# Performance work log

Measured on AMD Instinct MI355X. Metric: run time of the kernel, lower is better.

Reference implementation:

```python
import jax, jax.numpy as jnp
import numpy as np

N_TOKENS = 4096
EMBED = 2048
D_ATTN = 2048


def setup_inputs() -> dict:
    key = jax.random.key(0)
    k1, k2, k3, k4 = jax.random.split(key, 4)
    # torch.rand -> uniform [0,1); keeps scores positive so the multiplicative
    # -inf mask acts as a clean causal mask (faithful to original behavior).
    token_embeddings = jax.random.uniform(k1, (N_TOKENS, EMBED), dtype=jnp.float32)
    W_Q = jax.random.uniform(k2, (EMBED, D_ATTN), dtype=jnp.float32)
    W_K = jax.random.uniform(k3, (EMBED, D_ATTN), dtype=jnp.float32)
    W_V = jax.random.uniform(k4, (EMBED, D_ATTN), dtype=jnp.float32)
    return {"token_embeddings": token_embeddings, "W_Q": W_Q, "W_K": W_K, "W_V": W_V}


def reference(token_embeddings, W_Q, W_K, W_V):
    n = token_embeddings.shape[0]
    d = W_Q.shape[1]
    # mask: 1 on/below diagonal, -inf strictly above (multiplicative, as in source)
    neg_inf = jnp.float32(-jnp.inf)
    mask = jnp.tril(jnp.ones((n, n), dtype=jnp.float32)) + jnp.triu(
        jnp.full((n, n), neg_inf, dtype=jnp.float32), k=1
    )
    Q = token_embeddings @ W_Q          # (n, d)
    K = token_embeddings @ W_K          # (n, d)
    V = token_embeddings @ W_V          # (n, d)
    scores = (Q @ K.T) * mask           # (n, n); upper tri -> -inf (scores > 0)
    scores = scores / jnp.sqrt(jnp.float32(d))
    attn = jax.nn.softmax(scores, axis=-1)
    return attn @ V                     # (n, d)
```

## Files before the change

### kernel.cpp

```cpp
#include <hip/hip_runtime.h>
#include <hip/hip_bf16.h>
#include <cstdint>
#include <cstddef>
#include <cmath>

#define N_TOK 4096
#define EMB   2048
#define DATT  2048

typedef __attribute__((ext_vector_type(8))) short short8;
typedef __attribute__((ext_vector_type(4))) short shortx4;
typedef __attribute__((ext_vector_type(4))) float f32x4;

#define MFMA(a, b, c) __builtin_amdgcn_mfma_f32_16x16x32_bf16(a, b, c, 0, 0, 0)

__device__ __forceinline__ short f2bs(float f) {
  __hip_bfloat16 h = __float2bfloat16(f);
  return __builtin_bit_cast(short, h);
}
__device__ __forceinline__ float bs2f(short s) {
  return __uint_as_float(((unsigned)(unsigned short)s) << 16);
}
__device__ __forceinline__ float ldin(const void* p, size_t i, int isbf) {
  if (isbf) {
    unsigned short u = ((const unsigned short*)p)[i];
    return __uint_as_float(((unsigned int)u) << 16);
  }
  return ((const float*)p)[i];
}

__device__ __forceinline__ size_t swz(int r, int c, int kdim) {
  return ((size_t)((r >> 7) * (kdim >> 3) + (c >> 3)) << 10) +
         (size_t)((r & 127) << 3) + (c & 7);
}

__device__ __forceinline__ void gl16(const short* g, short* l) {
  __builtin_amdgcn_global_load_lds(
      (const __attribute__((address_space(1))) unsigned int*)(const void*)g,
      (__attribute__((address_space(3))) unsigned int*)(void*)l, 16, 0, 0);
}

template <bool THREE>
__device__ __forceinline__ void gemm_core(const short* Ah, const short* Al,
                                          const short* Bh, const short* Bl,
                                          int chunks, int apan, int bpan,
                                          int kmax, short* lds,
                                          f32x4 acc[4][4]) {
  const int NSL = THREE ? 4 : 2;
  int tid = threadIdx.x;
  int lane = tid & 63;
  int wave = tid >> 6;
  int ln = lane & 15, quad = lane >> 4;
  int wm = (wave >> 1) * 64, wn = (wave & 1) * 64;
  int wofs = wave * 512;

  auto stage = [&](int b, int k0) {
    size_t ao = ((size_t)(apan * chunks + (k0 >> 3))) << 10;
    size_t bo = ((size_t)(bpan * chunks + (k0 >> 3))) << 10;
    short* base = lds + b * NSL * 4096;
    const short* sa = Ah + ao + tid * 8;
    const short* sb = Bh + bo + tid * 8;
    gl16(sa,        base + wofs);
    gl16(sa + 2048, base + wofs + 2048);
    gl16(sb,        base + 4096 + wofs);
    gl16(sb + 2048, base + 4096 + wofs + 2048);
    if (THREE) {
      const short* sal = Al + ao + tid * 8;
      const short* sbl = Bl + bo + tid * 8;
      gl16(sal,        base + 8192 + wofs);
      gl16(sal + 2048, base + 8192 + wofs + 2048);
      gl16(sbl,        base + 12288 + wofs);
      gl16(sbl + 2048, base + 12288 + wofs + 2048);
    }
  };

  stage(0, 0);
  int cur = 0;
  int abase = quad * 1024 + (wm + ln) * 8;
  int bbase = quad * 1024 + (wn + ln) * 8;
  for (int k0 = 0; k0 < kmax; k0 += 32) {
    __syncthreads();
    if (k0 + 32 < kmax) stage(cur ^ 1, k0 + 32);
    const short* B0 = lds + cur * NSL * 4096;
    short8 fah[4], fbh[4];
#pragma unroll
    for (int i = 0; i < 4; ++i) fah[i] = *(const short8*)(B0 + abase + i * 128);
#pragma unroll
    for (int j = 0; j < 4; ++j) fbh[j] = *(const short8*)(B0 + 4096 + bbase + j * 128);
    if (THREE) {
      short8 fal[4], fbl[4];
#pragma unroll
      for (int i = 0; i < 4; ++i) fal[i] = *(const short8*)(B0 + 8192 + abase + i * 128);
#pragma unroll
      for (int j = 0; j < 4; ++j) fbl[j] = *(const short8*)(B0 + 12288 + bbase + j * 128);
#pragma unroll
      for (int j = 0; j < 4; ++j)
#pragma unroll
        for (int i = 0; i < 4; ++i) {
          acc[i][j] = MFMA(fah[i], fbh[j], acc[i][j]);
          acc[i][j] = MFMA(fah[i], fbl[j], acc[i][j]);
          acc[i][j] = MFMA(fal[i], fbh[j], acc[i][j]);
        }
    } else {
#pragma unroll
      for (int j = 0; j < 4; ++j)
#pragma unroll
        for (int i = 0; i < 4; ++i) acc[i][j] = MFMA(fah[i], fbh[j], acc[i][j]);
    }
    cur ^= 1;
  }
}

template <int AP, int BP>
__device__ __forceinline__ void gemm8(const short* __restrict__ Ah,
                                      const short* __restrict__ Al,
                                      const short* __restrict__ Bh,
                                      const short* __restrict__ Bl,
                                      int chunks, int apan, int bpan,
                                      int kmax, short* lds, f32x4 acc[4][4]) {
  constexpr int ASZ = AP * 4096;
  constexpr int BSZ = BP * 4096;
  constexpr int OAL = ASZ;
  constexpr int OBH = 2 * ASZ;
  constexpr int OBL = 2 * ASZ + BSZ;
  constexpr int BUF = 2 * ASZ + 2 * BSZ;
  constexpr int NNW = BP * 2;
  int tid = threadIdx.x;
  int lane = tid & 63, wave = tid >> 6;
  int ln = lane & 15, quad = lane >> 4;
  int wm = (wave / NNW) * 64, wn = (wave % NNW) * 64;
  int nt = kmax >> 5;

  auto sp = [&](int b, int t, int p) {
    short* base = lds + b * BUF;
    const short* g;
    short* l;
    if (p < AP)               { g = Ah + (((size_t)(apan + p) * chunks + (t << 2)) << 10);          l = base + p * 4096; }
    else if (p < 2 * AP)      { int q = p - AP;      g = Al + (((size_t)(apan + q) * chunks + (t << 2)) << 10); l = base + OAL + q * 4096; }
    else if (p < 2 * AP + BP) { int q = p - 2 * AP;  g = Bh + (((size_t)(bpan + q) * chunks + (t << 2)) << 10); l = base + OBH + q * 4096; }
    else                      { int q = p - 2 * AP - BP; g = Bl + (((size_t)(bpan + q) * chunks + (t << 2)) << 10); l = base + OBL + q * 4096; }
    gl16(g + tid * 8, l + wave * 512);
  };

#pragma unroll
  for (int p = 0; p < 6; ++p) sp(0, 0, p);
  if (nt > 1) {
#pragma unroll
    for (int p = 0; p < 6; ++p) sp(1, 1, p);
  }

  int abase = (wm & 128) * 32 + quad * 1024 + ((wm & 64) + ln) * 8;
  int bbase = (wn & 128) * 32 + quad * 1024 + ((wn & 64) + ln) * 8;
  int bi = 0;
  for (int t = 0; t < nt; ++t) {
    if (t + 1 < nt) asm volatile("s_waitcnt vmcnt(6)" ::: "memory");
    else            asm volatile("s_waitcnt vmcnt(0)" ::: "memory");
    __builtin_amdgcn_s_barrier();
    __builtin_amdgcn_sched_barrier(0);

    const short* L = lds + bi * BUF;
    int pi = bi + 2; if (pi > 2) pi -= 3;
    bool pf = (t + 2 < nt);

    short8 bh[4], bl[4];
#pragma unroll
    for (int j = 0; j < 4; ++j) {
      bh[j] = *(const short8*)(L + OBH + bbase + j * 128);
      bl[j] = *(const short8*)(L + OBL + bbase + j * 128);
    }
#pragma unroll
    for (int i = 0; i < 4; ++i) {
      short8 ah = *(const short8*)(L + abase + i * 128);
      short8 al = *(const short8*)(L + OAL + abase + i * 128);
      if (pf) {
        if (i == 0)      { sp(pi, t + 2, 0); sp(pi, t + 2, 1); }
        else if (i == 1) { sp(pi, t + 2, 2); sp(pi, t + 2, 3); }
        else if (i == 2) { sp(pi, t + 2, 4); }
        else             { sp(pi, t + 2, 5); }
      }
      __builtin_amdgcn_s_setprio(1);
#pragma unroll
      for (int j = 0; j < 4; ++j) {
        acc[i][j] = MFMA(ah, bh[j], acc[i][j]);
        acc[i][j] = MFMA(ah, bl[j], acc[i][j]);
        acc[i][j] = MFMA(al, bh[j], acc[i][j]);
      }
      __builtin_amdgcn_s_setprio(0);
    }
    ++bi; if (bi > 2) bi = 0;
  }
}

__device__ __forceinline__ void gemm1d2(const short* __restrict__ Ah,
                                        const short* __restrict__ Bh,
                                        int chunks, int apan, int bpan,
                                        int kmax, short* lds, f32x4 acc[4][4]) {
  int tid = threadIdx.x;
  int lane = tid & 63, wave = tid >> 6;
  int ln = lane & 15, quad = lane >> 4;
  int wm = (wave >> 1) * 64, wn = (wave & 1) * 64;
  int wofs = wave * 512;
  int nt = kmax >> 5;

  auto stage = [&](int b, int t) {
    size_t ao = ((size_t)(apan * chunks + (t << 2))) << 10;
    size_t bo = ((size_t)(bpan * chunks + (t << 2))) << 10;
    short* base = lds + b * 8192;
    gl16(Ah + ao + tid * 8,        base + wofs);
    gl16(Ah + ao + 2048 + tid * 8, base + wofs + 2048);
    gl16(Bh + bo + tid * 8,        base + 4096 + wofs);
    gl16(Bh + bo + 2048 + tid * 8, base + 4096 + wofs + 2048);
  };
  stage(0, 0);
  if (nt > 1) stage(1, 1);

  int abase = quad * 1024 + (wm + ln) * 8;
  int bbase = quad * 1024 + (wn + ln) * 8;
  int bi = 0;
  for (int t = 0; t < nt; ++t) {
    if (t + 1 < nt) asm volatile("s_waitcnt vmcnt(4)" ::: "memory");
    else            asm volatile("s_waitcnt vmcnt(0)" ::: "memory");
    __builtin_amdgcn_s_barrier();
    __builtin_amdgcn_sched_barrier(0);
    int pi = bi + 2; if (pi > 2) pi -= 3;
    if (t + 2 < nt) stage(pi, t + 2);
    const short* L = lds + bi * 8192;
    short8 fah[4], fbh[4];
#pragma unroll
    for (int i = 0; i < 4; ++i) fah[i] = *(const short8*)(L + abase + i * 128);
#pragma unroll
    for (int j = 0; j < 4; ++j) fbh[j] = *(const short8*)(L + 4096 + bbase + j * 128);
#pragma unroll
    for (int j = 0; j < 4; ++j)
#pragma unroll
      for (int i = 0; i < 4; ++i) acc[i][j] = MFMA(fah[i], fbh[j], acc[i][j]);
    ++bi; if (bi > 2) bi = 0;
  }
}

__global__ void k_sniff(const void* x, int* flag) {
  if (threadIdx.x == 0 && blockIdx.x == 0) {
    const unsigned short* u = (const unsigned short*)x;
    int bf = 1;
    for (int i = 0; i < 256; ++i) {
      unsigned short v = u[i];
      if ((v & 0x8000u) || ((v & 0x7FFFu) >= 0x3F80u)) { bf = 0; break; }
    }
    *flag = bf;
  }
}

__global__ __launch_bounds__(256) void k_xbar(const void* X, float* xbar,
                                              const int* flagp) {
  int isbf = *flagp;
  int e = blockIdx.x * 256 + threadIdx.x;
  float s = 0.f;
  for (int r = 0; r < 256; ++r) s += ldin(X, (size_t)r * EMB + e, isbf);
  xbar[e] = s * (1.f / 256.f);
}

__global__ __launch_bounds__(256) void k_split_x(const void* X, short* Xh, short* Xl,
                                                 const int* flagp) {
  int isbf = *flagp;
  size_t base = ((size_t)blockIdx.x * 256 + threadIdx.x) * 4;
  int r = (int)(base >> 11), c = (int)(base & 2047);
  shortx4 h, l;
#pragma unroll
  for (int u = 0; u < 4; ++u) {
    float x = ldin(X, base + u, isbf);
    short hh = f2bs(x);
    h[u] = hh;
    l[u] = f2bs(x - bs2f(hh));
  }
  size_t o = swz(r, c, EMB);
  *(shortx4*)(Xh + o) = h;
  *(shortx4*)(Xl + o) = l;
}

__global__ __launch_bounds__(256) void k_transpose_split(const void* W, short* Wth,
                                                         short* Wtl, int R, int C,
                                                         const int* flagp, int wlo) {
  __shared__ float T[64][65];
  int isbf = *flagp;
  int r0 = blockIdx.y * 64, c0 = blockIdx.x * 64;
  int tid = threadIdx.x;
#pragma unroll
  for (int it = 0; it < 16; ++it) {
    int idx = tid + it * 256;
    int row = idx >> 6, col = idx & 63;
    T[row][col] = ldin(W, (size_t)(r0 + row) * C + c0 + col, isbf);
  }
  __syncthreads();
#pragma unroll
  for (int it = 0; it < 16; ++it) {
    int idx = tid + it * 256;
    int row = idx >> 6, col = idx & 63;
    float x = T[col][row];
    short h = f2bs(x);
    size_t o = swz(c0 + row, r0 + col, R);
    Wth[o] = h;
    if (wlo) Wtl[o] = f2bs(x - bs2f(h));
  }
}

__global__ __launch_bounds__(256) void k_kbar(const short* Wth, const short* Wtl,
                                              const float* xbar, float* kbar) {
  int d = blockIdx.x;
  float s = 0.f;
  for (int e = threadIdx.x; e < EMB; e += 256) {
    size_t o = swz(d, e, EMB);
    s += xbar[e] * (bs2f(Wth[o]) + bs2f(Wtl[o]));
  }
  __shared__ float red[4];
#pragma unroll
  for (int off = 32; off > 0; off >>= 1) s += __shfl_down(s, off);
  if ((threadIdx.x & 63) == 0) red[threadIdx.x >> 6] = s;
  __syncthreads();
  if (threadIdx.x == 0) kbar[d] = red[0] + red[1] + red[2] + red[3];
}

__global__ __launch_bounds__(512, 2) void k_proj3(const short* Ah, const short* Al,
                                                  const short* Bh, const short* Bl,
                                                  short* Ch, short* Cl,
                                                  const float* bias) {
  __shared__ short lds[3 * 24576];
  int bid = blockIdx.x;
  int s = ((bid & 7) << 5) | (bid >> 3);
  int row0 = (s >> 4) << 8, col0 = (s & 15) << 7;
  f32x4 acc[4][4] = {};
  gemm8<2, 1>(Ah, Al, Bh, Bl, EMB >> 3, row0 >> 7, col0 >> 7, EMB, lds, acc);
  int tid = threadIdx.x;
  int wave = tid >> 6, lane = tid & 63;
  int ln = lane & 15, quad = lane >> 4;
  int wm = (wave >> 1) * 64, wn = (wave & 1) * 64;
#pragma unroll
  for (int i = 0; i < 4; ++i)
#pragma unroll
    for (int j = 0; j < 4; ++j)
#pragma unroll
      for (int r = 0; r < 4; ++r) {
        int row = row0 + wm + i * 16 + quad * 4 + r;
        int col = col0 + wn + j * 16 + ln;
        float x = acc[i][j][r];
        if (bias) x -= bias[col];
        short h = f2bs(x);
        size_t o = swz(row, col, DATT);
        Ch[o] = h;
        Cl[o] = f2bs(x - bs2f(h));
      }
}

__global__ __launch_bounds__(256, 3) void k_proj1(const short* Ah, const short* Bh,
                                                  short* Ch) {
  __shared__ short lds[3 * 8192];
  int bid = blockIdx.x;
  int s = ((bid & 7) << 6) | (bid >> 3);
  int row0 = (s >> 5) << 7, col0 = (s & 31) << 7;
  f32x4 acc[4][4] = {};
  gemm1d2(Ah, Bh, EMB >> 3, row0 >> 7, col0 >> 7, EMB, lds, acc);
  int tid = threadIdx.x;
  int wave = tid >> 6, lane = tid & 63;
  int ln = lane & 15, quad = lane >> 4;
  int wm = (wave >> 1) * 64, wn = (wave & 1) * 64;
#pragma unroll
  for (int i = 0; i < 4; ++i)
#pragma unroll
    for (int j = 0; j < 4; ++j)
#pragma unroll
      for (int r = 0; r < 4; ++r) {
        int row = row0 + wm + i * 16 + quad * 4 + r;
        int col = col0 + wn + j * 16 + ln;
        Ch[swz(row, col, N_TOK)] = f2bs(acc[i][j][r]);
      }
}

__global__ __launch_bounds__(256, 2) void k_score3(const short* Qh, const short* Ql,
                                                   const short* Kh, const short* Kl,
                                                   float* S) {
  int bi0 = blockIdx.x;
  int bi = (bi0 & 7) * 66 + (bi0 >> 3);
  int by = (int)((sqrtf(8.f * (float)bi + 1.f) - 1.f) * 0.5f);
  while ((by + 1) * (by + 2) / 2 <= bi) ++by;
  while (by * (by + 1) / 2 > bi) --by;
  int bx = bi - by * (by + 1) / 2;
  __shared__ short lds[2 * 16384];
  f32x4 acc[4][4] = {};
  gemm_core<true>(Qh, Ql, Kh, Kl, DATT >> 3, by, bx, DATT, lds, acc);
  int row0 = by * 128, col0 = bx * 128;
  int tid = threadIdx.x;
  int wave = tid >> 6, lane = tid & 63;
  int ln = lane & 15, quad = lane >> 4;
  int wm = (wave >> 1) * 64, wn = (wave & 1) * 64;
  const float scale = 0.022097086912079608f;
  if (bx < by) {
#pragma unroll
    for (int i = 0; i < 4; ++i)
#pragma unroll
      for (int j = 0; j < 4; ++j)
#pragma unroll
        for (int r = 0; r < 4; ++r) {
          int row = row0 + wm + i * 16 + quad * 4 + r;
          int col = col0 + wn + j * 16 + ln;
          S[(size_t)row * N_TOK + col] = acc[i][j][r] * scale;
        }
  } else {
#pragma unroll
    for (int i = 0; i < 4; ++i)
#pragma unroll
      for (int j = 0; j < 4; ++j)
#pragma unroll
        for (int r = 0; r < 4; ++r) {
          int row = row0 + wm + i * 16 + quad * 4 + r;
          int col = col0 + wn + j * 16 + ln;
          if (col <= row) S[(size_t)row * N_TOK + col] = acc[i][j][r] * scale;
        }
  }
}

__global__ __launch_bounds__(256) void k_softmax(const float* S, short* P) {
  int i = blockIdx.x;
  const float* row = S + (size_t)i * N_TOK;
  int len = i + 1;
  int tid = threadIdx.x;
  __shared__ float red[4];
  float m = -3.402823466e38f;
  for (int j = tid; j < len; j += 256) m = fmaxf(m, row[j]);
#pragma unroll
  for (int off = 32; off > 0; off >>= 1) m = fmaxf(m, __shfl_down(m, off));
  if ((tid & 63) == 0) red[tid >> 6] = m;
  __syncthreads();
  m = fmaxf(fmaxf(red[0], red[1]), fmaxf(red[2], red[3]));
  __syncthreads();
  float s = 0.f;
  for (int j = tid; j < len; j += 256) s += __expf(row[j] - m);
#pragma unroll
  for (int off = 32; off > 0; off >>= 1) s += __shfl_down(s, off);
  if ((tid & 63) == 0) red[tid >> 6] = s;
  __syncthreads();
  s = red[0] + red[1] + red[2] + red[3];
  float inv = 1.f / s;
  size_t rbase = ((size_t)(i >> 7) * (N_TOK >> 3) << 10) + (size_t)((i & 127) << 3);
  for (int j = tid; j < len; j += 256)
    P[rbase + ((size_t)(j >> 3) << 10) + (j & 7)] = f2bs(__expf(row[j] - m) * inv);
  int fillend = (len + 127) & ~127;
  for (int j = len + tid; j < fillend; j += 256)
    P[rbase + ((size_t)(j >> 3) << 10) + (j & 7)] = 0;
}

__global__ __launch_bounds__(256, 3) void k_out(const short* Ph, const short* Vh,
                                                void* Co, const int* flagp) {
  __shared__ short lds[3 * 8192];
  int bid = blockIdx.x;
  int half = bid >> 8;
  int r = bid & 255;
  int s = ((r & 7) << 5) | (r >> 3);
  int bb = s >> 4;
  int band = half ? bb : (31 - bb);
  int row0 = band << 7, col0 = (s & 15) << 7;
  f32x4 acc[4][4] = {};
  gemm1d2(Ph, Vh, N_TOK >> 3, row0 >> 7, col0 >> 7, row0 + 128, lds, acc);
  int isbf = *flagp;
  int tid = threadIdx.x;
  int wave = tid >> 6, lane = tid & 63;
  int ln = lane & 15, quad = lane >> 4;
  int wm = (wave >> 1) * 64, wn = (wave & 1) * 64;
#pragma unroll
  for (int i = 0; i < 4; ++i)
#pragma unroll
    for (int j = 0; j < 4; ++j)
#pragma unroll
      for (int r2 = 0; r2 < 4; ++r2) {
        int row = row0 + wm + i * 16 + quad * 4 + r2;
        int col = col0 + wn + j * 16 + ln;
        size_t idx = (size_t)row * DATT + col;
        if (isbf) ((__hip_bfloat16*)Co)[idx] = __float2bfloat16(acc[i][j][r2]);
        else      ((float*)Co)[idx] = acc[i][j][r2];
      }
}

extern "C" void kernel_launch(void* const* d_in, const int* in_sizes, int n_in,
                              void* d_out, int out_size, void* d_ws, size_t ws_size,
                              hipStream_t stream) {
  const void* X  = d_in[0];
  const void* WQ = d_in[1];
  const void* WK = d_in[2];
  const void* WV = d_in[3];

  float* ws   = (float*)d_ws;
  int*   flag = (int*)d_ws;
  float* xbar = ws + 256;
  float* kbar = ws + 2560;
  short* p0   = (short*)(ws + 16384);
  const size_t M8 = (size_t)N_TOK * DATT;
  const size_t M4 = (size_t)EMB * DATT;
  short* Xh  = p0;
  short* Xl  = Xh + M8;
  short* Wth = Xl + M8;
  short* Wtl = Wth + M4;
  float* S   = (float*)p0;
  short* Qh  = p0 + 4 * M8;
  short* Ql  = Qh + M8;
  short* Kh  = Ql + M8;
  short* Kl  = Kh + M8;
  short* Vt  = Kl + M8;
  short* P   = Qh;

  dim3 blk(256);
  dim3 blk512(512);

  k_sniff<<<1, 64, 0, stream>>>(X, flag);
  k_xbar<<<EMB / 256, blk, 0, stream>>>(X, xbar, flag);
  k_split_x<<<(N_TOK * EMB) / 1024, blk, 0, stream>>>(X, Xh, Xl, flag);

  dim3 gt(DATT / 64, EMB / 64);

  k_transpose_split<<<gt, blk, 0, stream>>>(WQ, Wth, Wtl, EMB, DATT, flag, 1);
  k_proj3<<<dim3(256), blk512, 0, stream>>>(Xh, Xl, Wth, Wtl, Qh, Ql, nullptr);
  k_transpose_split<<<gt, blk, 0, stream>>>(WK, Wth, Wtl, EMB, DATT, flag, 1);
  k_kbar<<<DATT, blk, 0, stream>>>(Wth, Wtl, xbar, kbar);
  k_proj3<<<dim3(256), blk512, 0, stream>>>(Xh, Xl, Wth, Wtl, Kh, Kl, kbar);
  k_transpose_split<<<gt, blk, 0, stream>>>(WV, Wth, nullptr, EMB, DATT, flag, 0);
  k_proj1<<<dim3(512), blk, 0, stream>>>(Wth, Xh, Vt);

  k_score3<<<dim3(528), blk, 0, stream>>>(Qh, Ql, Kh, Kl, S);

  k_softmax<<<dim3(N_TOK), blk, 0, stream>>>(S, P);

  k_out<<<dim3(512), blk, 0, stream>>>(P, Vt, d_out, flag);
}
```

Before: 647.9 us.

## Fuse V projection into score kernel and pack causal scores into triangular buffer

Merges the V projection GEMM and the causal QK^T score GEMM into one launch of 1040 blocks, so the two independent GEMMs fill the GPU together instead of running back to back. Scores now go into a packed lower-triangular block layout instead of a full NxN float matrix, which shrinks the score buffer and lets it sit beside the V weights in the workspace. Softmax reads rows at the matching packed offsets. The fused kernel runs at the 2-blocks-per-CU launch bound of the score GEMM and shares its larger LDS allocation, so the V projection part loses the occupancy of 3 it had before.

After: 617.1 us. 4.8% less time.

```diff
diff --git a/kernel.cpp b/kernel.cpp
--- a/kernel.cpp
+++ b/kernel.cpp
@@ -350,49 +350,58 @@
       }
 }
 
-__global__ __launch_bounds__(256, 3) void k_proj1(const short* Ah, const short* Bh,
-                                                  short* Ch) {
-  __shared__ short lds[3 * 8192];
+__global__ __launch_bounds__(256, 2) void k_score_pv(
+    const short* Qh, const short* Ql, const short* Kh, const short* Kl,
+    float* Spk, const short* Wvt, const short* Xh, short* Vt) {
+  __shared__ short lds[2 * 16384];
   int bid = blockIdx.x;
-  int s = ((bid & 7) << 6) | (bid >> 3);
-  int row0 = (s >> 5) << 7, col0 = (s & 31) << 7;
-  f32x4 acc[4][4] = {};
-  gemm1d2(Ah, Bh, EMB >> 3, row0 >> 7, col0 >> 7, EMB, lds, acc);
   int tid = threadIdx.x;
   int wave = tid >> 6, lane = tid & 63;
   int ln = lane & 15, quad = lane >> 4;
   int wm = (wave >> 1) * 64, wn = (wave & 1) * 64;
-#pragma unroll
-  for (int i = 0; i < 4; ++i)
-#pragma unroll
-    for (int j = 0; j < 4; ++j)
-#pragma unroll
-      for (int r = 0; r < 4; ++r) {
-        int row = row0 + wm + i * 16 + quad * 4 + r;
-        int col = col0 + wn + j * 16 + ln;
-        Ch[swz(row, col, N_TOK)] = f2bs(acc[i][j][r]);
-      }
-}
-
-__global__ __launch_bounds__(256, 2) void k_score3(const short* Qh, const short* Ql,
-                                                   const short* Kh, const short* Kl,
-                                                   float* S) {
-  int bi0 = blockIdx.x;
-  int bi = (bi0 & 7) * 66 + (bi0 >> 3);
-  int by = (int)((sqrtf(8.f * (float)bi + 1.f) - 1.f) * 0.5f);
-  while ((by + 1) * (by + 2) / 2 <= bi) ++by;
-  while (by * (by + 1) / 2 > bi) --by;
-  int bx = bi - by * (by + 1) / 2;
-  __shared__ short lds[2 * 16384];
-  f32x4 acc[4][4] = {};
-  gemm_core<true>(Qh, Ql, Kh, Kl, DATT >> 3, by, bx, DATT, lds, acc);
-  int row0 = by * 128, col0 = bx * 128;
-  int tid = threadIdx.x;
-  int wave = tid >> 6, lane = tid & 63;
-  int ln = lane & 15, quad = lane >> 4;
-  int wm = (wave >> 1) * 64, wn = (wave & 1) * 64;
-  const float scale = 0.022097086912079608f;
-  if (bx < by) {
+
+  if (bid < 528) {
+    int bi = (bid & 7) * 66 + (bid >> 3);
+    int by = (int)((sqrtf(8.f * (float)bi + 1.f) - 1.f) * 0.5f);
+    while ((by + 1) * (by + 2) / 2 <= bi) ++by;
+    while (by * (by + 1) / 2 > bi) --by;
+    int bx = bi - by * (by + 1) / 2;
+    f32x4 acc[4][4] = {};
+    gemm_core<true>(Qh, Ql, Kh, Kl, DATT >> 3, by, bx, DATT, lds, acc);
+    int row0 = by * 128, col0 = bx * 128;
+    const float scale = 0.022097086912079608f;
+    size_t base_b = (size_t)16384 * (size_t)(by * (by + 1) / 2);
+    int rstride = 128 * (by + 1);
+    if (bx < by) {
+#pragma unroll
+      for (int i = 0; i < 4; ++i)
+#pragma unroll
+        for (int j = 0; j < 4; ++j)
+#pragma unroll
+          for (int r = 0; r < 4; ++r) {
+            int rr = wm + i * 16 + quad * 4 + r;
+            int col = col0 + wn + j * 16 + ln;
+            Spk[base_b + (size_t)rr * rstride + col] = acc[i][j][r] * scale;
+          }
+    } else {
+#pragma unroll
+      for (int i = 0; i < 4; ++i)
+#pragma unroll
+        for (int j = 0; j < 4; ++j)
+#pragma unroll
+          for (int r = 0; r < 4; ++r) {
+            int rr = wm + i * 16 + quad * 4 + r;
+            int col = col0 + wn + j * 16 + ln;
+            if (col <= row0 + rr)
+              Spk[base_b + (size_t)rr * rstride + col] = acc[i][j][r] * scale;
+          }
+    }
+  } else {
+    int pid = bid - 528;
+    int s = ((pid & 7) << 6) | (pid >> 3);
+    int row0 = (s >> 5) << 7, col0 = (s & 31) << 7;
+    f32x4 acc[4][4] = {};
+    gemm1d2(Wvt, Xh, EMB >> 3, row0 >> 7, col0 >> 7, EMB, lds, acc);
 #pragma unroll
     for (int i = 0; i < 4; ++i)
 #pragma unroll
@@ -401,25 +410,16 @@
         for (int r = 0; r < 4; ++r) {
           int row = row0 + wm + i * 16 + quad * 4 + r;
           int col = col0 + wn + j * 16 + ln;
-          S[(size_t)row * N_TOK + col] = acc[i][j][r] * scale;
+          Vt[swz(row, col, N_TOK)] = f2bs(acc[i][j][r]);
         }
-  } else {
-#pragma unroll
-    for (int i = 0; i < 4; ++i)
-#pragma unroll
-      for (int j = 0; j < 4; ++j)
-#pragma unroll
-        for (int r = 0; r < 4; ++r) {
-          int row = row0 + wm + i * 16 + quad * 4 + r;
-          int col = col0 + wn + j * 16 + ln;
-          if (col <= row) S[(size_t)row * N_TOK + col] = acc[i][j][r] * scale;
-        }
-  }
-}
-
-__global__ __launch_bounds__(256) void k_softmax(const float* S, short* P) {
+  }
+}
+
+__global__ __launch_bounds__(256) void k_softmax(const float* Spk, short* P) {
   int i = blockIdx.x;
-  const float* row = S + (size_t)i * N_TOK;
+  int b = i >> 7;
+  const float* row = Spk + (size_t)16384 * (size_t)(b * (b + 1) / 2)
+                         + (size_t)(i & 127) * (128 * (b + 1));
   int len = i + 1;
   int tid = threadIdx.x;
   __shared__ float red[4];
@@ -497,7 +497,8 @@
   short* Xl  = Xh + M8;
   short* Wth = Xl + M8;
   short* Wtl = Wth + M4;
-  float* S   = (float*)p0;
+  float* Spk = (float*)(p0 + M8);
+  short* Wvt = p0 + 4 * M8 - M4;
   short* Qh  = p0 + 4 * M8;
   short* Ql  = Qh + M8;
   short* Kh  = Ql + M8;
@@ -519,12 +520,11 @@
   k_transpose_split<<<gt, blk, 0, stream>>>(WK, Wth, Wtl, EMB, DATT, flag, 1);
   k_kbar<<<DATT, blk, 0, stream>>>(Wth, Wtl, xbar, kbar);
   k_proj3<<<dim3(256), blk512, 0, stream>>>(Xh, Xl, Wth, Wtl, Kh, Kl, kbar);
-  k_transpose_split<<<gt, blk, 0, stream>>>(WV, Wth, nullptr, EMB, DATT, flag, 0);
-  k_proj1<<<dim3(512), blk, 0, stream>>>(Wth, Xh, Vt);
-
-  k_score3<<<dim3(528), blk, 0, stream>>>(Qh, Ql, Kh, Kl, S);
-
-  k_softmax<<<dim3(N_TOK), blk, 0, stream>>>(S, P);
+  k_transpose_split<<<gt, blk, 0, stream>>>(WV, Wvt, nullptr, EMB, DATT, flag, 0);
+
+  k_score_pv<<<dim3(1040), blk, 0, stream>>>(Qh, Ql, Kh, Kl, Spk, Wvt, Xh, Vt);
+
+  k_softmax<<<dim3(N_TOK), blk, 0, stream>>>(Spk, P);
 
   k_out<<<dim3(512), blk, 0, stream>>>(P, Vt, d_out, flag);
 }
```
